# Kernel tuning notes

Measured on AMD Instinct MI355X. Metric: run time of the kernel, lower is better.

The kernel has to match this reference:

```python
import jax, jax.numpy as jnp
import numpy as np

B, S, H, L, NH, DH, FF = 64, 256, 768, 12, 12, 64, 3072
V, MAXP, NTYPE, NI, NS = 30522, 512, 2, 10, 64


def setup_inputs() -> dict:
    key = jax.random.key(0)
    ks = iter(jax.random.split(key, 40))
    n = lambda shp, s=0.02: jax.random.normal(next(ks), shp, jnp.float32) * s
    inp = {
        'input_ids': jax.random.randint(next(ks), (B, S), 0, V),
        'attention_mask': jnp.ones((B, S), jnp.int32),
        'token_type_ids': jnp.zeros((B, S), jnp.int32),
        'intent_labels': jax.random.randint(next(ks), (B,), 0, NI),
        'slot_labels': jax.random.randint(next(ks), (B, S), 0, NS),
        'word_emb': n((V, H)), 'pos_emb': n((MAXP, H)), 'type_emb': n((NTYPE, H)),
        'emb_ln_g': jnp.ones((H,)), 'emb_ln_b': jnp.zeros((H,)),
        'Wq': n((L, H, H)), 'bq': jnp.zeros((L, H)),
        'Wk': n((L, H, H)), 'bk': jnp.zeros((L, H)),
        'Wv': n((L, H, H)), 'bv': jnp.zeros((L, H)),
        'Wo': n((L, H, H)), 'bo': jnp.zeros((L, H)),
        'ln1_g': jnp.ones((L, H)), 'ln1_b': jnp.zeros((L, H)),
        'W1': n((L, H, FF)), 'b1': jnp.zeros((L, FF)),
        'W2': n((L, FF, H)), 'b2': jnp.zeros((L, H)),
        'ln2_g': jnp.ones((L, H)), 'ln2_b': jnp.zeros((L, H)),
        'Wi': n((H, NI)), 'bi': jnp.zeros((NI,)),
        'Ws': n((H, NS)), 'bs': jnp.zeros((NS,)),
        'crf_start': n((NS,), 0.1), 'crf_end': n((NS,), 0.1),
        'crf_trans': n((NS, NS), 0.1),
    }
    return inp


def _ln(x, g, b):
    m = x.mean(-1, keepdims=True)
    v = jnp.square(x - m).mean(-1, keepdims=True)
    return (x - m) * jax.lax.rsqrt(v + 1e-12) * g + b


def _forward(params, input_ids, attention_mask, token_type_ids, intent_labels, slot_labels):
    (word_emb, pos_emb, type_emb, emb_ln_g, emb_ln_b,
     Wq, bq, Wk, bk, Wv, bv, Wo, bo, ln1_g, ln1_b,
     W1, b1, W2, b2, ln2_g, ln2_b,
     Wi, bi, Ws, bs, crf_start, crf_end, crf_trans) = params
    Bn, Sn = input_ids.shape
    Hn = word_emb.shape[1]
    dh = Hn // NH
    # BERT embeddings (dropout is identity in eval)
    x = word_emb[input_ids] + pos_emb[:Sn][None] + type_emb[token_type_ids]
    x = _ln(x, emb_ln_g, emb_ln_b)
    bias = (1.0 - attention_mask.astype(x.dtype))[:, None, None, :] * -1e9  # [B,1,1,S]

    def layer(h, p):
        wq, cq, wk, ck, wv, cv, wo, co, g1, d1, w1, e1, w2, e2, g2, d2 = p
        q = (h @ wq + cq).reshape(Bn, Sn, NH, dh)
        k = (h @ wk + ck).reshape(Bn, Sn, NH, dh)
        v = (h @ wv + cv).reshape(Bn, Sn, NH, dh)
        sc = jnp.einsum('bqnd,bknd->bnqk', q, k) / jnp.sqrt(jnp.float32(dh)) + bias
        a = jax.nn.softmax(sc, axis=-1)
        ctx = jnp.einsum('bnqk,bknd->bqnd', a, v).reshape(Bn, Sn, Hn)
        h2 = _ln(h + ctx @ wo + co, g1, d1)
        ff = jax.nn.gelu(h2 @ w1 + e1, approximate=False)
        return _ln(h2 + ff @ w2 + e2, g2, d2), None

    x, _ = jax.lax.scan(layer, x, (Wq, bq, Wk, bk, Wv, bv, Wo, bo,
                                   ln1_g, ln1_b, W1, b1, W2, b2, ln2_g, ln2_b))
    intent_logits = x[:, 0, :] @ Wi + bi           # [B, NI]
    slot_logits = x @ Ws + bs                      # [B, S, NS]
    # intent cross-entropy (mean over batch)
    lp = jax.nn.log_softmax(intent_logits, axis=-1)
    intent_loss = -jnp.take_along_axis(lp, intent_labels[:, None], axis=1).mean()
    # CRF log-likelihood
    mask = attention_mask.astype(slot_logits.dtype)
    em, tags = slot_logits, slot_labels
    t0 = tags[:, 0]
    score = crf_start[t0] + jnp.take_along_axis(em[:, 0, :], t0[:, None], axis=1)[:, 0]
    prev, cur = tags[:, :-1], tags[:, 1:]
    step_sc = crf_trans[prev, cur] + jnp.take_along_axis(em[:, 1:, :], cur[..., None], axis=2)[..., 0]
    score = score + (step_sc * mask[:, 1:]).sum(1)
    lengths = attention_mask.sum(1)
    last_tag = jnp.take_along_axis(tags, (lengths - 1)[:, None].astype(tags.dtype), axis=1)[:, 0]
    score = score + crf_end[last_tag]
    em_t = jnp.swapaxes(em, 0, 1)    # [S,B,C]
    mk_t = jnp.swapaxes(mask, 0, 1)  # [S,B]
    alpha0 = crf_start[None, :] + em_t[0]

    def crf_step(alpha, xs):
        e, m = xs
        nxt = jax.scipy.special.logsumexp(alpha[:, :, None] + crf_trans[None], axis=1) + e
        return jnp.where(m[:, None] > 0, nxt, alpha), None

    alpha, _ = jax.lax.scan(crf_step, alpha0, (em_t[1:], mk_t[1:]))
    logZ = jax.scipy.special.logsumexp(alpha + crf_end[None, :], axis=1)
    llh = score - logZ                # per-sequence log-likelihood
    crf_loss = -llh.mean()
    return intent_loss + 2.0 * crf_loss


def reference(input_ids, attention_mask, token_type_ids, intent_labels, slot_labels,
              word_emb, pos_emb, type_emb, emb_ln_g, emb_ln_b,
              Wq, bq, Wk, bk, Wv, bv, Wo, bo, ln1_g, ln1_b,
              W1, b1, W2, b2, ln2_g, ln2_b,
              Wi, bi, Ws, bs, crf_start, crf_end, crf_trans):
    params = (word_emb, pos_emb, type_emb, emb_ln_g, emb_ln_b,
              Wq, bq, Wk, bk, Wv, bv, Wo, bo, ln1_g, ln1_b,
              W1, b1, W2, b2, ln2_g, ln2_b,
              Wi, bi, Ws, bs, crf_start, crf_end, crf_trans)
    return _forward(params, input_ids, attention_mask, token_type_ids, intent_labels, slot_labels)
```

## Files before the change

kernel.cpp:

```cpp
#include <hip/hip_runtime.h>
#include <stdint.h>

typedef unsigned short u16;
typedef __attribute__((ext_vector_type(8))) short bh8;
typedef __attribute__((ext_vector_type(4))) float f4;

#define DEV static __device__ __forceinline__

DEV u16 f2bf(float f){ union{float f; uint32_t u;} v; v.f=f; uint32_t r=v.u + 0x7FFFu + ((v.u>>16)&1u); return (u16)(r>>16); }
DEV float bf2f(u16 u){ union{uint32_t u; float f;} v; v.u=((uint32_t)u)<<16; return v.f; }

DEV void mfma16(f4& d, bh8 a, bh8 b){
  d = __builtin_amdgcn_mfma_f32_16x16x32_bf16(a, b, d, 0, 0, 0);
}

DEV float gelu(float v){
  float x = v*0.70710678118f;
  float ax = fabsf(x);
  float tt = 1.0f/(1.0f + 0.3275911f*ax);
  float y = 1.0f - (((((1.061405429f*tt - 1.453152027f)*tt) + 1.421413741f)*tt
                     - 0.284496736f)*tt + 0.254829592f)*tt*__expf(-ax*ax);
  float e = (x<0.f)? -y : y;
  return 0.5f*v*(1.0f+e);
}

#define GLD16(g,l) __builtin_amdgcn_global_load_lds( \
    (__attribute__((address_space(1))) void*)(void*)(g), \
    (__attribute__((address_space(3))) void*)(void*)(l), 16, 0, 0)

struct GemmP { const u16* A; const u16* B; int K; void* C; int ldc;
               const float* b0; const float* b1; const float* b2; const u16* res; };

template<int EPI>
DEV void epi_store(const GemmP& p, int gr, int gc, float v){
  if(EPI==0){
    const float* bp = (gc<768)? p.b0 : (gc<1536? p.b1 : p.b2);
    const int bc = (gc<768)? gc : (gc<1536? gc-768 : gc-1536);
    ((u16*)p.C)[(size_t)gr*p.ldc + gc] = f2bf(v + bp[bc]);
  } else if(EPI==1){
    v += p.b0[gc] + bf2f(p.res[(size_t)gr*p.ldc + gc]);
    ((u16*)p.C)[(size_t)gr*p.ldc + gc] = f2bf(v);
  } else if(EPI==2){
    ((u16*)p.C)[(size_t)gr*p.ldc + gc] = f2bf(gelu(v + p.b0[gc]));
  } else {
    v += (gc<64)? p.b0[gc] : 0.f;
    ((float*)p.C)[(size_t)gr*p.ldc + gc] = v;
  }
}

template<int EPI>
__global__ __launch_bounds__(512)
void gemm256(GemmP p){
  extern __shared__ char smem[];
  const int t=threadIdx.x, l=t&63, w=t>>6;
  const int wr=w>>2, wc=w&3;
  const int m0=blockIdx.x*256, n0=blockIdx.y*256;
  const int K=p.K, NT=K>>6;
  const int fl=l&15, fh=l>>4;

  const int r0=(w*1024+l*16)>>7;
  const int cs=(((l&7)^(l>>3))<<4);
  const char* gA0 = (const char*)p.A + ((size_t)(m0+r0)*K)*2 + cs;
  const char* gB0 = (const char*)p.B + ((size_t)(n0+r0)*K)*2 + cs;
  const size_t rowblk = (size_t)64*K*2;
  char* dA = smem + w*1024;
  char* dB = smem + 32768 + w*1024;

  #define SG_A(T,h,buf) do{ const char* _s=gA0 + (size_t)(T)*128 + (size_t)(h)*2*rowblk; \
    char* _d=dA+(buf)*65536+(h)*16384; GLD16(_s,_d); GLD16(_s+rowblk,_d+8192); }while(0)
  #define SG_B(T,h,buf) do{ const char* _s=gB0 + (size_t)(T)*128 + (size_t)(h)*2*rowblk; \
    char* _d=dB+(buf)*65536+(h)*16384; GLD16(_s,_d); GLD16(_s+rowblk,_d+8192); }while(0)

  int oB[4][2], oA[8][2];
#pragma unroll
  for(int nf=0;nf<4;nf++){ const int rw=wc*64+nf*16+fl;
#pragma unroll
    for(int ks=0;ks<2;ks++) oB[nf][ks] = 32768 + rw*128 + ((ks*64+fh*16) ^ ((rw&7)<<4)); }
#pragma unroll
  for(int mf=0;mf<8;mf++){ const int rw=wr*128+mf*16+fl;
#pragma unroll
    for(int ks=0;ks<2;ks++) oA[mf][ks] = rw*128 + ((ks*64+fh*16) ^ ((rw&7)<<4)); }

  f4 acc[8][4] = {};
  bh8 bf_[4][2], af_[2][2];

  #define MFMA_Q(q) do{ \
    __builtin_amdgcn_s_setprio(1); \
    _Pragma("unroll") \
    for(int j=0;j<2;j++) \
      _Pragma("unroll") \
      for(int nf=0;nf<4;nf++){ mfma16(acc[2*(q)+j][nf], af_[j][0], bf_[nf][0]); \
                               mfma16(acc[2*(q)+j][nf], af_[j][1], bf_[nf][1]); } \
    __builtin_amdgcn_s_setprio(0); }while(0)

  #define WAIT_LGKM do{ asm volatile("s_waitcnt lgkmcnt(0)":::"memory"); \
    __builtin_amdgcn_sched_barrier(0); }while(0)

  SG_A(0,0,0); SG_A(0,1,0); SG_B(0,0,0); SG_B(0,1,0);
  if(NT>1){ SG_B(1,0,1); SG_B(1,1,1);
            asm volatile("s_waitcnt vmcnt(4)":::"memory"); }
  else    { asm volatile("s_waitcnt vmcnt(0)":::"memory"); }
  __builtin_amdgcn_s_barrier();

  for(int T=0; T<NT; ++T){
    const int cur=T&1, nxt=cur^1;
    const char* sb = smem + (cur<<16);
    if(T+1<NT){ SG_A(T+1,0,nxt); SG_A(T+1,1,nxt); }
#pragma unroll
    for(int nf=0;nf<4;nf++){ bf_[nf][0]=*(const bh8*)(sb+oB[nf][0]); bf_[nf][1]=*(const bh8*)(sb+oB[nf][1]); }
    af_[0][0]=*(const bh8*)(sb+oA[0][0]); af_[0][1]=*(const bh8*)(sb+oA[0][1]);
    af_[1][0]=*(const bh8*)(sb+oA[1][0]); af_[1][1]=*(const bh8*)(sb+oA[1][1]);
    __builtin_amdgcn_s_barrier();
    WAIT_LGKM;
    MFMA_Q(0);
    __builtin_amdgcn_s_barrier();
    if(T+2<NT) SG_B(T+2,0,cur);
    af_[0][0]=*(const bh8*)(sb+oA[2][0]); af_[0][1]=*(const bh8*)(sb+oA[2][1]);
    af_[1][0]=*(const bh8*)(sb+oA[3][0]); af_[1][1]=*(const bh8*)(sb+oA[3][1]);
    __builtin_amdgcn_s_barrier();
    WAIT_LGKM;
    MFMA_Q(1);
    __builtin_amdgcn_s_barrier();
    if(T+2<NT) SG_B(T+2,1,cur);
    af_[0][0]=*(const bh8*)(sb+oA[4][0]); af_[0][1]=*(const bh8*)(sb+oA[4][1]);
    af_[1][0]=*(const bh8*)(sb+oA[5][0]); af_[1][1]=*(const bh8*)(sb+oA[5][1]);
    __builtin_amdgcn_s_barrier();
    WAIT_LGKM;
    MFMA_Q(2);
    __builtin_amdgcn_s_barrier();
    af_[0][0]=*(const bh8*)(sb+oA[6][0]); af_[0][1]=*(const bh8*)(sb+oA[6][1]);
    af_[1][0]=*(const bh8*)(sb+oA[7][0]); af_[1][1]=*(const bh8*)(sb+oA[7][1]);
    if(T+2<NT)      asm volatile("s_waitcnt vmcnt(4)":::"memory");
    else if(T+1<NT) asm volatile("s_waitcnt vmcnt(0)":::"memory");
    __builtin_amdgcn_s_barrier();
    WAIT_LGKM;
    MFMA_Q(3);
    __builtin_amdgcn_s_barrier();
  }
  #undef SG_A
  #undef SG_B
  #undef MFMA_Q
  #undef WAIT_LGKM

  const int lr=fh*4;
#pragma unroll
  for(int m=0;m<8;m++)
#pragma unroll
  for(int n=0;n<4;n++)
#pragma unroll
  for(int r=0;r<4;r++){
    epi_store<EPI>(p, m0 + wr*128 + m*16 + lr + r, n0 + wc*64 + n*16 + fl, acc[m][n][r]);
  }
}

template<int EPI>
__global__ __launch_bounds__(256)
void gemm_bt(GemmP p){
  __shared__ __align__(16) u16 As[128*64];
  __shared__ __align__(16) u16 Bs[128*64];
  const int t=threadIdx.x, l=t&63, w=t>>6, wr=w>>1, wc=w&1;
  const int fl=l&15, fh=l>>4;
  const int m0=blockIdx.x*128, n0=blockIdx.y*128;
  const int K=p.K, NT=K>>6;
  const int srow=t>>3;
  const int cs=(((t&7) ^ (srow&7))<<4);
  const char* gA = (const char*)p.A + ((size_t)(m0+srow)*K)*2 + cs;
  const char* gB = (const char*)p.B + ((size_t)(n0+srow)*K)*2 + cs;
  const size_t r32 = (size_t)32*K*2;
  char* dA = (char*)As + t*16;
  char* dB = (char*)Bs + t*16;

  int oA2[4][2], oB2[4][2];
#pragma unroll
  for(int mf=0;mf<4;mf++){ const int rw=wr*64+mf*16+fl;
#pragma unroll
    for(int ks=0;ks<2;ks++) oA2[mf][ks] = rw*128 + ((ks*64+fh*16) ^ ((rw&7)<<4)); }
#pragma unroll
  for(int nf=0;nf<4;nf++){ const int rw=wc*64+nf*16+fl;
#pragma unroll
    for(int ks=0;ks<2;ks++) oB2[nf][ks] = rw*128 + ((ks*64+fh*16) ^ ((rw&7)<<4)); }

  f4 acc[4][4] = {};
  for(int T=0; T<NT; ++T){
#pragma unroll
    for(int j=0;j<4;j++) GLD16(gA + (size_t)T*128 + j*r32, dA + j*4096);
#pragma unroll
    for(int j=0;j<4;j++) GLD16(gB + (size_t)T*128 + j*r32, dB + j*4096);
    __syncthreads();
    bh8 af[4][2], bfr[4][2];
#pragma unroll
    for(int mf=0;mf<4;mf++){ af[mf][0]=*(const bh8*)((const char*)As+oA2[mf][0]);
                             af[mf][1]=*(const bh8*)((const char*)As+oA2[mf][1]); }
#pragma unroll
    for(int nf=0;nf<4;nf++){ bfr[nf][0]=*(const bh8*)((const char*)Bs+oB2[nf][0]);
                             bfr[nf][1]=*(const bh8*)((const char*)Bs+oB2[nf][1]); }
#pragma unroll
    for(int ks=0;ks<2;ks++)
#pragma unroll
      for(int m=0;m<4;m++)
#pragma unroll
        for(int n=0;n<4;n++) mfma16(acc[m][n], af[m][ks], bfr[n][ks]);
    __syncthreads();
  }
  const int lr=fh*4;
#pragma unroll
  for(int m=0;m<4;m++)
#pragma unroll
  for(int n=0;n<4;n++)
#pragma unroll
  for(int r=0;r<4;r++){
    epi_store<EPI>(p, m0 + wr*64 + m*16 + lr + r, n0 + wc*64 + n*16 + fl, acc[m][n][r]);
  }
}

__global__ __launch_bounds__(256)
void attn_kernel(const u16* __restrict__ qkv, const int* __restrict__ amask, u16* __restrict__ ctx){
  __shared__ __align__(16) u16 Ks[256*64];
  __shared__ __align__(16) u16 Vt[64*256];
  __shared__ __align__(16) u16 Ps[4*64*64];
  __shared__ float biasS[256];
  const int t=threadIdx.x, l=t&63, w=t>>6;
  const int b=blockIdx.x/12, h=blockIdx.x%12;
  biasS[t] = (1.f - (float)amask[b*256+t]) * -1e9f;
  const u16* kb = qkv + ((size_t)b*256)*2304 + 768 + h*64;
  const u16* vb = kb + 768;
#pragma unroll
  for(int i=0;i<8;i++){
    const int c = t + i*256;
    const int row = c>>3, seg = c&7;
    uint4 kv = *(const uint4*)(kb + (size_t)row*2304 + seg*8);
    const int ba = row*128 + seg*16;
    *(uint4*)((char*)Ks + (ba ^ ((row&7)<<4))) = kv;
    uint4 vv = *(const uint4*)(vb + (size_t)row*2304 + seg*8);
    const u16* pv = (const u16*)&vv;
#pragma unroll
    for(int j=0;j<8;j++){
      const int d = seg*8+j;
      const int bb = d*512 + row*2;
      *(u16*)((char*)Vt + (bb ^ ((d&7)<<4))) = pv[j];
    }
  }
  bh8 aq[4][2];
  const u16* qb = qkv + ((size_t)b*256 + w*64)*2304 + h*64;
#pragma unroll
  for(int m=0;m<4;m++)
#pragma unroll
    for(int ks=0;ks<2;ks++)
      aq[m][ks] = *(const bh8*)(qb + (size_t)(m*16+(l&15))*2304 + ks*32 + (l>>4)*8);
  __syncthreads();
  float mrun[4][4], lrun[4][4];
  f4 o[4][4] = {};
#pragma unroll
  for(int m=0;m<4;m++)
#pragma unroll
    for(int r=0;r<4;r++){ mrun[m][r] = -3e38f; lrun[m][r]=0.f; }
  u16* Pw = Ps + w*4096;
  for(int kt=0;kt<4;kt++){
    f4 sacc[4][4] = {};
#pragma unroll
    for(int ks=0;ks<2;ks++)
#pragma unroll
      for(int n=0;n<4;n++){
        const int row = kt*64 + n*16 + (l&15);
        const int by = row*128 + ks*64 + (l>>4)*16;
        bh8 bk = *(const bh8*)((const char*)Ks + (by ^ ((row&7)<<4)));
#pragma unroll
        for(int m=0;m<4;m++) mfma16(sacc[m][n], aq[m][ks], bk);
      }
#pragma unroll
    for(int m=0;m<4;m++){
      float rmax[4] = {-3e38f,-3e38f,-3e38f,-3e38f};
#pragma unroll
      for(int n=0;n<4;n++){
        const float bi = biasS[kt*64 + n*16 + (l&15)];
#pragma unroll
        for(int r=0;r<4;r++){
          float sv = sacc[m][n][r]*0.125f + bi;
          sacc[m][n][r] = sv;
          rmax[r] = fmaxf(rmax[r], sv);
        }
      }
#pragma unroll
      for(int dd=1; dd<16; dd<<=1)
#pragma unroll
        for(int r=0;r<4;r++) rmax[r] = fmaxf(rmax[r], __shfl_xor(rmax[r], dd));
      float psum[4];
#pragma unroll
      for(int r=0;r<4;r++){
        const float mn = fmaxf(mrun[m][r], rmax[r]);
        const float corr = __expf(mrun[m][r] - mn);
        mrun[m][r] = mn;
        lrun[m][r] *= corr;
#pragma unroll
        for(int nd=0; nd<4; nd++) o[m][nd][r] *= corr;
        psum[r] = 0.f;
      }
#pragma unroll
      for(int n=0;n<4;n++)
#pragma unroll
        for(int r=0;r<4;r++){
          const float pvv = __expf(sacc[m][n][r] - mrun[m][r]);
          sacc[m][n][r] = pvv;
          psum[r] += pvv;
        }
#pragma unroll
      for(int dd=1; dd<16; dd<<=1)
#pragma unroll
        for(int r=0;r<4;r++) psum[r] += __shfl_xor(psum[r], dd);
#pragma unroll
      for(int r=0;r<4;r++) lrun[m][r] += psum[r];
#pragma unroll
      for(int n=0;n<4;n++)
#pragma unroll
        for(int r=0;r<4;r++){
          const int prow = m*16 + (l>>4)*4 + r;
          const int pcol = n*16 + (l&15);
          const int by = prow*128 + pcol*2;
          *(u16*)((char*)Pw + (by ^ ((prow&7)<<4))) = f2bf(sacc[m][n][r]);
        }
    }
#pragma unroll
    for(int ks=0;ks<2;ks++){
      bh8 ap[4];
#pragma unroll
      for(int m=0;m<4;m++){
        const int prow = m*16 + (l&15);
        const int by = prow*128 + (ks*32 + (l>>4)*8)*2;
        ap[m] = *(const bh8*)((const char*)Pw + (by ^ ((prow&7)<<4)));
      }
#pragma unroll
      for(int nd=0; nd<4; nd++){
        const int dR = nd*16 + (l&15);
        const int by = dR*512 + (kt*64 + ks*32 + (l>>4)*8)*2;
        bh8 bv = *(const bh8*)((const char*)Vt + (by ^ ((dR&7)<<4)));
#pragma unroll
        for(int m=0;m<4;m++) mfma16(o[m][nd], ap[m], bv);
      }
    }
  }
#pragma unroll
  for(int m=0;m<4;m++)
#pragma unroll
  for(int nd=0; nd<4; nd++)
#pragma unroll
  for(int r=0;r<4;r++){
    const int row = w*64 + m*16 + (l>>4)*4 + r;
    const float vv = o[m][nd][r] / lrun[m][r];
    ctx[((size_t)b*256 + row)*768 + h*64 + nd*16 + (l&15)] = f2bf(vv);
  }
}

__global__ void ln_kernel(const u16* __restrict__ in, const float* __restrict__ g,
                          const float* __restrict__ b, u16* __restrict__ out){
  const int row = blockIdx.x, t = threadIdx.x;
  __shared__ float red[8];
  const u16* rp = in + (size_t)row*768;
  float v[3]; float s=0.f, q=0.f;
#pragma unroll
  for(int i=0;i<3;i++){ float x = bf2f(rp[t + i*256]); v[i]=x; s+=x; q+=x*x; }
#pragma unroll
  for(int dd=1; dd<64; dd<<=1){ s += __shfl_xor(s,dd); q += __shfl_xor(q,dd); }
  if((t&63)==0){ red[t>>6]=s; red[4+(t>>6)]=q; }
  __syncthreads();
  s = red[0]+red[1]+red[2]+red[3];
  q = red[4]+red[5]+red[6]+red[7];
  const float mean = s*(1.f/768.f);
  float var = q*(1.f/768.f) - mean*mean; var = fmaxf(var, 0.f);
  const float rs = rsqrtf(var + 1e-12f);
  u16* op = out + (size_t)row*768;
#pragma unroll
  for(int i=0;i<3;i++){ const int hh=t+i*256; op[hh] = f2bf((v[i]-mean)*rs*g[hh] + b[hh]); }
}

__global__ void embed_ln(const int* __restrict__ ids, const int* __restrict__ tti,
    const float* __restrict__ we, const float* __restrict__ pe, const float* __restrict__ te,
    const float* __restrict__ g, const float* __restrict__ bb, u16* __restrict__ x){
  const int tok = blockIdx.x, t = threadIdx.x;
  __shared__ float red[8];
  const int id = ids[tok], tyid = tti[tok], s0 = tok & 255;
  float v[3]; float s=0.f,q=0.f;
#pragma unroll
  for(int i=0;i<3;i++){
    const int hh = t+i*256;
    float x0 = we[(size_t)id*768+hh] + pe[(size_t)s0*768+hh] + te[(size_t)tyid*768+hh];
    v[i]=x0; s+=x0; q+=x0*x0;
  }
#pragma unroll
  for(int dd=1; dd<64; dd<<=1){ s += __shfl_xor(s,dd); q += __shfl_xor(q,dd); }
  if((t&63)==0){ red[t>>6]=s; red[4+(t>>6)]=q; }
  __syncthreads();
  s = red[0]+red[1]+red[2]+red[3];
  q = red[4]+red[5]+red[6]+red[7];
  const float mean = s*(1.f/768.f);
  float var = q*(1.f/768.f) - mean*mean; var = fmaxf(var, 0.f);
  const float rs = rsqrtf(var + 1e-12f);
#pragma unroll
  for(int i=0;i<3;i++){ const int hh=t+i*256; x[(size_t)tok*768+hh] = f2bf((v[i]-mean)*rs*g[hh] + bb[hh]); }
}

__global__ void transpose_cvt(const float* __restrict__ src, u16* __restrict__ dst, int R, int C){
  __shared__ float sm[32][33];
  const int ntc = C>>5;
  const int tr = blockIdx.x/ntc, tc = blockIdx.x - tr*ntc;
  const int r0 = tr<<5, c0 = tc<<5;
  const int tx = threadIdx.x, ty2 = threadIdx.y;
#pragma unroll
  for(int i=0;i<4;i++) sm[ty2+i*8][tx] = src[(size_t)(r0+ty2+i*8)*C + c0+tx];
  __syncthreads();
#pragma unroll
  for(int i=0;i<4;i++) dst[(size_t)(c0+ty2+i*8)*R + r0+tx] = f2bf(sm[tx][ty2+i*8]);
}

__global__ void conv_layer(const float* __restrict__ Wq, const float* __restrict__ Wk,
    const float* __restrict__ Wv, const float* __restrict__ Wo,
    const float* __restrict__ W1, const float* __restrict__ W2, u16* __restrict__ Wt){
  __shared__ float sm[32][33];
  const int bid = blockIdx.x;
  const float* src; u16* dst; int R, C, tt;
  if(bid<2304){
    R=768; C=768; const int mi = bid/576; tt = bid - mi*576;
    src = (mi==0?Wq: mi==1?Wk: mi==2?Wv: Wo);
    dst = Wt + (size_t)mi*589824;
  } else if(bid<4608){ R=768; C=3072; tt=bid-2304; src=W1; dst=Wt+2359296; }
  else { R=3072; C=768; tt=bid-4608; src=W2; dst=Wt+4718592; }
  const int ntc=C>>5; const int tr=tt/ntc, tc=tt-tr*ntc;
  const int r0=tr<<5, c0=tc<<5, tx=threadIdx.x, ty2=threadIdx.y;
#pragma unroll
  for(int i=0;i<4;i++) sm[ty2+i*8][tx] = src[(size_t)(r0+ty2+i*8)*C + c0+tx];
  __syncthreads();
#pragma unroll
  for(int i=0;i<4;i++) dst[(size_t)(c0+ty2+i*8)*R + r0+tx] = f2bf(sm[tx][ty2+i*8]);
}

__global__ void intent_kernel(const u16* __restrict__ x, const float* __restrict__ Wi,
    const float* __restrict__ bi, const int* __restrict__ lab, float* __restrict__ parts){
  const int b = blockIdx.x, t = threadIdx.x;
  __shared__ float xs[768];
  __shared__ float lg[10];
  const u16* rp = x + ((size_t)b*256)*768;
#pragma unroll
  for(int i=0;i<3;i++) xs[t+i*256] = bf2f(rp[t+i*256]);
  __syncthreads();
  if(t<10){
    float s = bi[t];
    for(int k=0;k<768;k++) s += xs[k]*Wi[(size_t)k*10 + t];
    lg[t] = s;
  }
  __syncthreads();
  if(t==0){
    float m = lg[0];
    for(int j=1;j<10;j++) m = fmaxf(m, lg[j]);
    float se = 0.f;
    for(int j=0;j<10;j++) se += expf(lg[j]-m);
    parts[b] = (logf(se) + m) - lg[lab[b]];
  }
}

__global__ __launch_bounds__(64)
void crf_kernel(const float* __restrict__ em, const int* __restrict__ tags,
    const int* __restrict__ amask, const float* __restrict__ cs, const float* __restrict__ ce,
    const float* __restrict__ tr, float* __restrict__ parts){
  const int b = blockIdx.x, j = threadIdx.x;
  const float* eb = em + (size_t)b*256*128;
  const int* tg = tags + b*256;
  const int* mk = amask + b*256;
  __shared__ __align__(16) float aS[64];
  float Etr[64];
#pragma unroll
  for(int i=0;i<64;i++) Etr[i] = __expf(tr[i*64 + j]);
  float sc = 0.f; int len = 0;
  for(int s=j+1; s<256; s+=64){
    const int pv = tg[s-1], cu = tg[s];
    sc += (tr[pv*64+cu] + eb[(size_t)s*128+cu]) * (float)mk[s];
  }
  for(int s=j; s<256; s+=64) len += mk[s];
#pragma unroll
  for(int dd=1; dd<64; dd<<=1){ sc += __shfl_xor(sc,dd); len += __shfl_xor(len,dd); }
  const int t0 = tg[0];
  float score = sc + cs[t0] + eb[t0] + ce[tg[len-1]];
  float a = __expf(cs[j] + eb[j]);
  float logc = 0.f;
  float em_s = eb[128 + j];
  int   mk_s = mk[1];
  for(int s=1; s<256; s++){
    const int sn = (s<255)? s+1 : s;
    const float em_n = eb[(size_t)sn*128 + j];
    const int   mk_n = mk[sn];
    aS[j] = a;
    __syncthreads();
    float acc0=0.f, acc1=0.f, acc2=0.f, acc3=0.f;
    const float4* ap = (const float4*)aS;
#pragma unroll
    for(int q2=0;q2<16;q2++){
      const float4 av = ap[q2];
      acc0 += av.x*Etr[4*q2+0];
      acc1 += av.y*Etr[4*q2+1];
      acc2 += av.z*Etr[4*q2+2];
      acc3 += av.w*Etr[4*q2+3];
    }
    __syncthreads();
    const float nxt = ((acc0+acc1)+(acc2+acc3)) * __expf(em_s);
    a = (mk_s > 0) ? nxt : a;
    if((s&7)==7){
      const float c = __shfl(a, 0);
      logc += __logf(c);
      a *= (1.f/c);
    }
    em_s = em_n; mk_s = mk_n;
  }
  float v2 = logf(a) + logc + ce[j];
  float am2 = v2;
#pragma unroll
  for(int dd=1; dd<64; dd<<=1) am2 = fmaxf(am2, __shfl_xor(am2,dd));
  float se = __expf(v2 - am2);
#pragma unroll
  for(int dd=1; dd<64; dd<<=1) se += __shfl_xor(se,dd);
  if(j==0) parts[64+b] = (logf(se)+am2) - score;
}

__global__ void final_reduce(const float* __restrict__ parts, float* __restrict__ out){
  const int t = threadIdx.x;
  float a = parts[t], c = parts[64+t];
#pragma unroll
  for(int dd=1; dd<64; dd<<=1){ a += __shfl_xor(a,dd); c += __shfl_xor(c,dd); }
  if(t==0) out[0] = a*(1.f/64.f) + 2.f*c*(1.f/64.f);
}

extern "C" void kernel_launch(void* const* d_in, const int* in_sizes, int n_in,
                              void* d_out, int out_size, void* d_ws, size_t ws_size,
                              hipStream_t stream){
  (void)in_sizes; (void)n_in; (void)out_size;
  const int* ids   = (const int*)d_in[0];
  const int* amask = (const int*)d_in[1];
  const int* tti   = (const int*)d_in[2];
  const int* ilab  = (const int*)d_in[3];
  const int* slab  = (const int*)d_in[4];
  const float* we  = (const float*)d_in[5];
  const float* pe  = (const float*)d_in[6];
  const float* te  = (const float*)d_in[7];
  const float* eg  = (const float*)d_in[8];
  const float* ebt = (const float*)d_in[9];
  const float* Wq  = (const float*)d_in[10];
  const float* bq  = (const float*)d_in[11];
  const float* Wk  = (const float*)d_in[12];
  const float* bkk = (const float*)d_in[13];
  const float* Wv  = (const float*)d_in[14];
  const float* bvv = (const float*)d_in[15];
  const float* Wo  = (const float*)d_in[16];
  const float* bo  = (const float*)d_in[17];
  const float* l1g = (const float*)d_in[18];
  const float* l1b = (const float*)d_in[19];
  const float* W1  = (const float*)d_in[20];
  const float* b1  = (const float*)d_in[21];
  const float* W2  = (const float*)d_in[22];
  const float* b2  = (const float*)d_in[23];
  const float* l2g = (const float*)d_in[24];
  const float* l2b = (const float*)d_in[25];
  const float* Wi  = (const float*)d_in[26];
  const float* bi  = (const float*)d_in[27];
  const float* Wsp = (const float*)d_in[28];
  const float* bs  = (const float*)d_in[29];
  const float* cs  = (const float*)d_in[30];
  const float* ce  = (const float*)d_in[31];
  const float* ctr = (const float*)d_in[32];

  char* ws = (char*)d_ws;
  size_t off = 0;
  auto alloc = [&](size_t bytes)->void*{ void* p = ws + off; off += (bytes+255)&~(size_t)255; return p; };
  u16* x     = (u16*)alloc(16384ull*768*2);
  u16* h2    = (u16*)alloc(16384ull*768*2);
  u16* y     = (u16*)alloc(16384ull*768*2);
  u16* qkv   = (u16*)alloc(16384ull*2304*2);
  u16* cf    = (u16*)alloc(16384ull*3072*2);
  u16* Wt    = (u16*)alloc(7077888ull*2);
  u16* WsT   = (u16*)alloc(128ull*768*2);
  float* slots = (float*)alloc(16384ull*128*4);
  float* parts = (float*)alloc(512);
  if(off > ws_size) return;

  (void)hipFuncSetAttribute((const void*)gemm256<0>, hipFuncAttributeMaxDynamicSharedMemorySize, 131072);
  (void)hipFuncSetAttribute((const void*)gemm256<2>, hipFuncAttributeMaxDynamicSharedMemorySize, 131072);

  dim3 T256(256), T512(512), T328(32,8);
  embed_ln<<<dim3(16384), T256, 0, stream>>>(ids, tti, we, pe, te, eg, ebt, x);
  transpose_cvt<<<dim3(48), T328, 0, stream>>>(Wsp, WsT, 768, 64);
  for(int L=0; L<12; L++){
    const size_t oH = (size_t)L*768*768, oF = (size_t)L*768*3072;
    conv_layer<<<dim3(6912), T328, 0, stream>>>(Wq+oH, Wk+oH, Wv+oH, Wo+oH, W1+oF, W2+oF, Wt);
    GemmP pq{ x, Wt, 768, qkv, 2304, bq+L*768, bkk+L*768, bvv+L*768, nullptr };
    gemm256<0><<<dim3(64,9), T512, 131072, stream>>>(pq);
    attn_kernel<<<dim3(768), T256, 0, stream>>>(qkv, amask, cf);
    GemmP po{ cf, Wt+1769472, 768, y, 768, bo+L*768, nullptr, nullptr, x };
    gemm_bt<1><<<dim3(128,6), T256, 0, stream>>>(po);
    ln_kernel<<<dim3(16384), T256, 0, stream>>>(y, l1g+L*768, l1b+L*768, h2);
    GemmP p1{ h2, Wt+2359296, 768, cf, 3072, b1+L*3072, nullptr, nullptr, nullptr };
    gemm256<2><<<dim3(64,12), T512, 131072, stream>>>(p1);
    GemmP p2{ cf, Wt+4718592, 3072, y, 768, b2+L*768, nullptr, nullptr, h2 };
    gemm_bt<1><<<dim3(128,6), T256, 0, stream>>>(p2);
    ln_kernel<<<dim3(16384), T256, 0, stream>>>(y, l2g+L*768, l2b+L*768, x);
  }
  GemmP psl{ x, WsT, 768, slots, 128, bs, nullptr, nullptr, nullptr };
  gemm_bt<3><<<dim3(128,1), T256, 0, stream>>>(psl);
  intent_kernel<<<dim3(64), T256, 0, stream>>>(x, Wi, bi, ilab, parts);
  crf_kernel<<<dim3(64), dim3(64), 0, stream>>>(slots, slab, amask, cs, ce, ctr, parts);
  final_reduce<<<dim3(1), dim3(64), 0, stream>>>(parts, (float*)d_out);
}
```

Baseline: 6.043 ms.

## Route N=768 GEMMs through 256-tile kernel, unroll pipeline, shrink gemm_bt K-step

The Wo and W2 projections move from the 128x128 gemm_bt kernel to the 256-wide pipelined gemm256 kernel with the residual epilogue, launched on a 64x3 grid. The gemm256 main loop is unrolled by two with alternating fragment register sets to break register dependencies across quarter-steps. The wait for outstanding loads moves after the last MFMA group. gemm_bt now uses a 32-wide K step with smaller LDS tiles, though after this change it only serves the small slot projection. The 64x3 grid gives only 192 workgroups, which may underfill the GPU. The unrolled loop assumes NT is even, which holds for K=768 and 3072.

```diff
diff --git a/kernel.cpp b/kernel.cpp
--- a/kernel.cpp
+++ b/kernel.cpp
@@ -82,19 +82,54 @@
     for(int ks=0;ks<2;ks++) oA[mf][ks] = rw*128 + ((ks*64+fh*16) ^ ((rw&7)<<4)); }
 
   f4 acc[8][4] = {};
-  bh8 bf_[4][2], af_[2][2];
-
-  #define MFMA_Q(q) do{ \
+  bh8 bfA[4][2], bfB[4][2], afA[2][2], afB[2][2];
+
+  #define MFMA_Q(q, AF, BF) do{ \
     __builtin_amdgcn_s_setprio(1); \
     _Pragma("unroll") \
     for(int j=0;j<2;j++) \
       _Pragma("unroll") \
-      for(int nf=0;nf<4;nf++){ mfma16(acc[2*(q)+j][nf], af_[j][0], bf_[nf][0]); \
-                               mfma16(acc[2*(q)+j][nf], af_[j][1], bf_[nf][1]); } \
+      for(int nf=0;nf<4;nf++){ mfma16(acc[2*(q)+j][nf], AF[j][0], BF[nf][0]); \
+                               mfma16(acc[2*(q)+j][nf], AF[j][1], BF[nf][1]); } \
     __builtin_amdgcn_s_setprio(0); }while(0)
 
   #define WAIT_LGKM do{ asm volatile("s_waitcnt lgkmcnt(0)":::"memory"); \
     __builtin_amdgcn_sched_barrier(0); }while(0)
+
+  #define TILE(T, CUR, BF) do{ \
+    const char* sb = smem + ((CUR)<<16); \
+     \
+    if((T)+1<NT){ SG_A((T)+1,0,(CUR)^1); SG_A((T)+1,1,(CUR)^1); } \
+    _Pragma("unroll") \
+    for(int nf=0;nf<4;nf++){ BF[nf][0]=*(const bh8*)(sb+oB[nf][0]); BF[nf][1]=*(const bh8*)(sb+oB[nf][1]); } \
+    afA[0][0]=*(const bh8*)(sb+oA[0][0]); afA[0][1]=*(const bh8*)(sb+oA[0][1]); \
+    afA[1][0]=*(const bh8*)(sb+oA[1][0]); afA[1][1]=*(const bh8*)(sb+oA[1][1]); \
+    __builtin_amdgcn_s_barrier(); WAIT_LGKM; \
+    MFMA_Q(0, afA, BF); \
+    __builtin_amdgcn_s_barrier(); \
+     \
+    if((T)+2<NT) SG_B((T)+2,0,(CUR)); \
+    afB[0][0]=*(const bh8*)(sb+oA[2][0]); afB[0][1]=*(const bh8*)(sb+oA[2][1]); \
+    afB[1][0]=*(const bh8*)(sb+oA[3][0]); afB[1][1]=*(const bh8*)(sb+oA[3][1]); \
+    __builtin_amdgcn_s_barrier(); WAIT_LGKM; \
+    MFMA_Q(1, afB, BF); \
+    __builtin_amdgcn_s_barrier(); \
+     \
+    if((T)+2<NT) SG_B((T)+2,1,(CUR)); \
+    afA[0][0]=*(const bh8*)(sb+oA[4][0]); afA[0][1]=*(const bh8*)(sb+oA[4][1]); \
+    afA[1][0]=*(const bh8*)(sb+oA[5][0]); afA[1][1]=*(const bh8*)(sb+oA[5][1]); \
+    __builtin_amdgcn_s_barrier(); WAIT_LGKM; \
+    MFMA_Q(2, afA, BF); \
+    __builtin_amdgcn_s_barrier(); \
+     \
+    afB[0][0]=*(const bh8*)(sb+oA[6][0]); afB[0][1]=*(const bh8*)(sb+oA[6][1]); \
+    afB[1][0]=*(const bh8*)(sb+oA[7][0]); afB[1][1]=*(const bh8*)(sb+oA[7][1]); \
+    __builtin_amdgcn_s_barrier(); WAIT_LGKM; \
+    MFMA_Q(3, afB, BF); \
+    if((T)+2<NT)      asm volatile("s_waitcnt vmcnt(4)":::"memory"); \
+    else if((T)+1<NT) asm volatile("s_waitcnt vmcnt(0)":::"memory"); \
+    __builtin_amdgcn_s_barrier(); \
+  }while(0)
 
   SG_A(0,0,0); SG_A(0,1,0); SG_B(0,0,0); SG_B(0,1,0);
   if(NT>1){ SG_B(1,0,1); SG_B(1,1,1);
@@ -102,41 +137,11 @@
   else    { asm volatile("s_waitcnt vmcnt(0)":::"memory"); }
   __builtin_amdgcn_s_barrier();
 
-  for(int T=0; T<NT; ++T){
-    const int cur=T&1, nxt=cur^1;
-    const char* sb = smem + (cur<<16);
-    if(T+1<NT){ SG_A(T+1,0,nxt); SG_A(T+1,1,nxt); }
-#pragma unroll
-    for(int nf=0;nf<4;nf++){ bf_[nf][0]=*(const bh8*)(sb+oB[nf][0]); bf_[nf][1]=*(const bh8*)(sb+oB[nf][1]); }
-    af_[0][0]=*(const bh8*)(sb+oA[0][0]); af_[0][1]=*(const bh8*)(sb+oA[0][1]);
-    af_[1][0]=*(const bh8*)(sb+oA[1][0]); af_[1][1]=*(const bh8*)(sb+oA[1][1]);
-    __builtin_amdgcn_s_barrier();
-    WAIT_LGKM;
-    MFMA_Q(0);
-    __builtin_amdgcn_s_barrier();
-    if(T+2<NT) SG_B(T+2,0,cur);
-    af_[0][0]=*(const bh8*)(sb+oA[2][0]); af_[0][1]=*(const bh8*)(sb+oA[2][1]);
-    af_[1][0]=*(const bh8*)(sb+oA[3][0]); af_[1][1]=*(const bh8*)(sb+oA[3][1]);
-    __builtin_amdgcn_s_barrier();
-    WAIT_LGKM;
-    MFMA_Q(1);
-    __builtin_amdgcn_s_barrier();
-    if(T+2<NT) SG_B(T+2,1,cur);
-    af_[0][0]=*(const bh8*)(sb+oA[4][0]); af_[0][1]=*(const bh8*)(sb+oA[4][1]);
-    af_[1][0]=*(const bh8*)(sb+oA[5][0]); af_[1][1]=*(const bh8*)(sb+oA[5][1]);
-    __builtin_amdgcn_s_barrier();
-    WAIT_LGKM;
-    MFMA_Q(2);
-    __builtin_amdgcn_s_barrier();
-    af_[0][0]=*(const bh8*)(sb+oA[6][0]); af_[0][1]=*(const bh8*)(sb+oA[6][1]);
-    af_[1][0]=*(const bh8*)(sb+oA[7][0]); af_[1][1]=*(const bh8*)(sb+oA[7][1]);
-    if(T+2<NT)      asm volatile("s_waitcnt vmcnt(4)":::"memory");
-    else if(T+1<NT) asm volatile("s_waitcnt vmcnt(0)":::"memory");
-    __builtin_amdgcn_s_barrier();
-    WAIT_LGKM;
-    MFMA_Q(3);
-    __builtin_amdgcn_s_barrier();
-  }
+  for(int T=0; T<NT; T+=2){
+    TILE(T,   0, bfA);
+    TILE(T+1, 1, bfB);
+  }
+  #undef TILE
   #undef SG_A
   #undef SG_B
   #undef MFMA_Q
@@ -156,50 +161,44 @@
 template<int EPI>
 __global__ __launch_bounds__(256)
 void gemm_bt(GemmP p){
-  __shared__ __align__(16) u16 As[128*64];
-  __shared__ __align__(16) u16 Bs[128*64];
+  __shared__ __align__(16) u16 As[128*32];
+  __shared__ __align__(16) u16 Bs[128*32];
   const int t=threadIdx.x, l=t&63, w=t>>6, wr=w>>1, wc=w&1;
   const int fl=l&15, fh=l>>4;
   const int m0=blockIdx.x*128, n0=blockIdx.y*128;
-  const int K=p.K, NT=K>>6;
-  const int srow=t>>3;
-  const int cs=(((t&7) ^ (srow&7))<<4);
+  const int K=p.K, NT=K>>5;
+  const int srow=t>>2;
+  const int cs=(((t&3) ^ (srow&3))<<4);
   const char* gA = (const char*)p.A + ((size_t)(m0+srow)*K)*2 + cs;
   const char* gB = (const char*)p.B + ((size_t)(n0+srow)*K)*2 + cs;
-  const size_t r32 = (size_t)32*K*2;
+  const size_t r64 = (size_t)64*K*2;
   char* dA = (char*)As + t*16;
   char* dB = (char*)Bs + t*16;
 
-  int oA2[4][2], oB2[4][2];
+  int oA2[4], oB2[4];
 #pragma unroll
   for(int mf=0;mf<4;mf++){ const int rw=wr*64+mf*16+fl;
-#pragma unroll
-    for(int ks=0;ks<2;ks++) oA2[mf][ks] = rw*128 + ((ks*64+fh*16) ^ ((rw&7)<<4)); }
+    oA2[mf] = rw*64 + ((fh ^ (rw&3))<<4); }
 #pragma unroll
   for(int nf=0;nf<4;nf++){ const int rw=wc*64+nf*16+fl;
-#pragma unroll
-    for(int ks=0;ks<2;ks++) oB2[nf][ks] = rw*128 + ((ks*64+fh*16) ^ ((rw&7)<<4)); }
+    oB2[nf] = rw*64 + ((fh ^ (rw&3))<<4); }
 
   f4 acc[4][4] = {};
   for(int T=0; T<NT; ++T){
-#pragma unroll
-    for(int j=0;j<4;j++) GLD16(gA + (size_t)T*128 + j*r32, dA + j*4096);
-#pragma unroll
-    for(int j=0;j<4;j++) GLD16(gB + (size_t)T*128 + j*r32, dB + j*4096);
+    GLD16(gA + (size_t)T*64, dA);
+    GLD16(gA + (size_t)T*64 + r64, dA + 4096);
+    GLD16(gB + (size_t)T*64, dB);
+    GLD16(gB + (size_t)T*64 + r64, dB + 4096);
     __syncthreads();
-    bh8 af[4][2], bfr[4][2];
-#pragma unroll
-    for(int mf=0;mf<4;mf++){ af[mf][0]=*(const bh8*)((const char*)As+oA2[mf][0]);
-                             af[mf][1]=*(const bh8*)((const char*)As+oA2[mf][1]); }
-#pragma unroll
-    for(int nf=0;nf<4;nf++){ bfr[nf][0]=*(const bh8*)((const char*)Bs+oB2[nf][0]);
-                             bfr[nf][1]=*(const bh8*)((const char*)Bs+oB2[nf][1]); }
-#pragma unroll
-    for(int ks=0;ks<2;ks++)
-#pragma unroll
-      for(int m=0;m<4;m++)
-#pragma unroll
-        for(int n=0;n<4;n++) mfma16(acc[m][n], af[m][ks], bfr[n][ks]);
+    bh8 af[4], bfr[4];
+#pragma unroll
+    for(int mf=0;mf<4;mf++) af[mf]=*(const bh8*)((const char*)As+oA2[mf]);
+#pragma unroll
+    for(int nf=0;nf<4;nf++) bfr[nf]=*(const bh8*)((const char*)Bs+oB2[nf]);
+#pragma unroll
+    for(int m=0;m<4;m++)
+#pragma unroll
+      for(int n=0;n<4;n++) mfma16(acc[m][n], af[m], bfr[n]);
     __syncthreads();
   }
   const int lr=fh*4;
@@ -579,6 +578,7 @@
   if(off > ws_size) return;
 
   (void)hipFuncSetAttribute((const void*)gemm256<0>, hipFuncAttributeMaxDynamicSharedMemorySize, 131072);
+  (void)hipFuncSetAttribute((const void*)gemm256<1>, hipFuncAttributeMaxDynamicSharedMemorySize, 131072);
   (void)hipFuncSetAttribute((const void*)gemm256<2>, hipFuncAttributeMaxDynamicSharedMemorySize, 131072);
 
   dim3 T256(256), T512(512), T328(32,8);
@@ -591,12 +591,12 @@
     gemm256<0><<<dim3(64,9), T512, 131072, stream>>>(pq);
     attn_kernel<<<dim3(768), T256, 0, stream>>>(qkv, amask, cf);
     GemmP po{ cf, Wt+1769472, 768, y, 768, bo+L*768, nullptr, nullptr, x };
-    gemm_bt<1><<<dim3(128,6), T256, 0, stream>>>(po);
+    gemm256<1><<<dim3(64,3), T512, 131072, stream>>>(po);
     ln_kernel<<<dim3(16384), T256, 0, stream>>>(y, l1g+L*768, l1b+L*768, h2);
     GemmP p1{ h2, Wt+2359296, 768, cf, 3072, b1+L*3072, nullptr, nullptr, nullptr };
     gemm256<2><<<dim3(64,12), T512, 131072, stream>>>(p1);
     GemmP p2{ cf, Wt+4718592, 3072, y, 768, b2+L*768, nullptr, nullptr, h2 };
-    gemm_bt<1><<<dim3(128,6), T256, 0, stream>>>(p2);
+    gemm256<1><<<dim3(64,3), T512, 131072, stream>>>(p2);
     ln_kernel<<<dim3(16384), T256, 0, stream>>>(y, l2g+L*768, l2b+L*768, x);
   }
   GemmP psl{ x, WsT, 768, slots, 128, bs, nullptr, nullptr, nullptr };
```

New measurement: 5.506 ms. -8.9%, faster.
